# Optimization experiments

Hardware: AMD Instinct MI355X
Metric: run time of the kernel (lower is better)

Reference implementation:

```python
import jax, jax.numpy as jnp
import numpy as np

NUM_CLASSES = 14
ATTN_DIM = 64
BN_EPS = 1e-5

def setup_inputs() -> dict:
    key = jax.random.key(0)
    ks = jax.random.split(key, 6)
    B, F = 16384, 2048
    C, D = NUM_CLASSES, ATTN_DIM
    std = 0.02
    return {
        "features": jax.random.normal(ks[0], (B, F), jnp.float32),
        "W_proj": jax.random.normal(ks[1], (F, F), jnp.float32) * std,
        "b_proj": jnp.zeros((F,), jnp.float32),
        "bn_gamma": jnp.ones((F,), jnp.float32),
        "bn_beta": jnp.zeros((F,), jnp.float32),
        "W_qk": jax.random.normal(ks[2], (C * 2 * D, F), jnp.float32) * std,
        "gamma": jax.random.normal(ks[3], (C,), jnp.float32) * 0.1,
        "W_fc": jax.random.normal(ks[4], (C, F), jnp.float32) * std,
        "b_fc": jnp.zeros((C,), jnp.float32),
    }

def reference(features, W_proj, b_proj, bn_gamma, bn_beta, W_qk, gamma, W_fc, b_fc):
    B = features.shape[0]
    C, D = NUM_CLASSES, ATTN_DIM
    # fc logits
    logits = features @ W_fc.T + b_fc  # [B, C]
    # projection: Linear -> BatchNorm1d (training-mode batch stats) -> ReLU
    h = features @ W_proj.T + b_proj  # [B, P]
    mu = jnp.mean(h, axis=0)
    var = jnp.var(h, axis=0)  # biased, as torch BN uses for normalization
    h = (h - mu) * jax.lax.rsqrt(var + BN_EPS) * bn_gamma + bn_beta
    h = jax.nn.relu(h)
    # per-class q, k
    qk = h @ W_qk.T  # [B, 2*C*D]
    q, k = jnp.split(qk, 2, axis=-1)
    q = q.reshape(B, C, D)
    k = k.reshape(B, C, D)
    attn = jnp.einsum("bcd,bed->bce", q, k)  # [B, C, C]
    diag = jnp.diagonal(attn, axis1=-2, axis2=-1)  # [B, C]
    attn = attn - diag[..., None]
    attn = attn / jnp.max(jnp.abs(attn), axis=-1, keepdims=True)
    corr = jnp.einsum("bce,be->bc", attn, jax.nn.sigmoid(logits))  # [B, C]
    return logits + gamma * corr
```

## Files before the change

### kernel.cpp

```cpp
#include <hip/hip_runtime.h>
#include <stdint.h>

#define BROWS 16384
#define FDIM  2048
#define NCLS  14
#define ADIM  64
#define NCAT  2176
#define QKN   1792

typedef __attribute__((ext_vector_type(8))) short bhalf8_t;
typedef __attribute__((ext_vector_type(4))) float f32x4_t;

__device__ __forceinline__ unsigned short f2bf(float f) {
  unsigned int u = __builtin_bit_cast(unsigned int, f);
  u += 0x7fffu + ((u >> 16) & 1u);
  return (unsigned short)(u >> 16);
}

__device__ __forceinline__ void gl_lds16(const void* g, void* l) {
  __builtin_amdgcn_global_load_lds(
      (const __attribute__((address_space(1))) unsigned int*)g,
      (__attribute__((address_space(3))) unsigned int*)l, 16, 0, 0);
}


__global__ void cast8_bf16(const float* __restrict__ src,
                           unsigned short* __restrict__ dst, int n8) {
  int t = blockIdx.x * 256 + threadIdx.x;
  if (t >= n8) return;
  const float4* s = (const float4*)src + 2 * (size_t)t;
  float4 a = s[0], b = s[1];
  bhalf8_t o;
  o[0] = f2bf(a.x); o[1] = f2bf(a.y); o[2] = f2bf(a.z); o[3] = f2bf(a.w);
  o[4] = f2bf(b.x); o[5] = f2bf(b.y); o[6] = f2bf(b.z); o[7] = f2bf(b.w);
  *((bhalf8_t*)dst + t) = o;
}

__global__ void build_wcat(const float* __restrict__ Wp, const float* __restrict__ Wf,
                           unsigned short* __restrict__ dst) {
  int row = blockIdx.x;
  int c8 = threadIdx.x * 8;
  const float* src = nullptr;
  if (row < 2048) src = Wp + (size_t)row * FDIM + c8;
  else if (row < 2048 + NCLS) src = Wf + (size_t)(row - 2048) * FDIM + c8;
  bhalf8_t o = {0,0,0,0,0,0,0,0};
  if (src) {
    float4 a = *(const float4*)src, b = *(const float4*)(src + 4);
    o[0] = f2bf(a.x); o[1] = f2bf(a.y); o[2] = f2bf(a.z); o[3] = f2bf(a.w);
    o[4] = f2bf(b.x); o[5] = f2bf(b.y); o[6] = f2bf(b.z); o[7] = f2bf(b.w);
  }
  *(bhalf8_t*)(dst + (size_t)row * FDIM + c8) = o;
}

__global__ void build_biascat(const float* __restrict__ bp, const float* __restrict__ bf,
                              float* __restrict__ dst) {
  int i = blockIdx.x * 256 + threadIdx.x;
  if (i >= NCAT) return;
  dst[i] = (i < 2048) ? bp[i] : ((i < 2048 + NCLS) ? bf[i - 2048] : 0.f);
}

__global__ __launch_bounds__(256) void gemm_bt(
    const unsigned short* __restrict__ A, const unsigned short* __restrict__ Bw,
    const float* __restrict__ bias, float* __restrict__ C,
    int K, int lda, int ldb, int ldc)
{
  __shared__ unsigned short lA[128 * 64];
  __shared__ unsigned short lB[128 * 64];
  const int tid = threadIdx.x;
  const int lane = tid & 63, wv = tid >> 6;
  const int m = lane & 15, quad = lane >> 4;
  const size_t rowBase = (size_t)blockIdx.x * 128;
  const size_t colBase = (size_t)blockIdx.y * 128;
  const int m0 = (wv >> 1) * 64, n0 = (wv & 1) * 64;

  f32x4_t acc[4][4];
#pragma unroll
  for (int i = 0; i < 4; ++i)
#pragma unroll
    for (int j = 0; j < 4; ++j) acc[i][j] = (f32x4_t){0.f, 0.f, 0.f, 0.f};

  int sS[4];
  size_t gA[4], gB[4];
#pragma unroll
  for (int i = 0; i < 4; ++i) {
    int s = ((i * 4 + wv) << 6) + lane;
    int r = s >> 3, qp = s & 7;
    int q = qp ^ (r & 7);
    sS[i] = s;
    gA[i] = (rowBase + r) * (size_t)lda + q * 8;
    gB[i] = (colBase + r) * (size_t)ldb + q * 8;
  }

  for (int kb = 0; kb < K; kb += 64) {
#pragma unroll
    for (int i = 0; i < 4; ++i) {
      gl_lds16(A + gA[i] + kb, &lA[sS[i] * 8]);
      gl_lds16(Bw + gB[i] + kb, &lB[sS[i] * 8]);
    }
    __syncthreads();
#pragma unroll
    for (int ks = 0; ks < 2; ++ks) {
      const int qc = ks * 4 + quad;
      bhalf8_t af[4], bf[4];
#pragma unroll
      for (int mi = 0; mi < 4; ++mi) {
        int r = m0 + mi * 16 + m;
        af[mi] = *(const bhalf8_t*)&lA[(r * 8 + (qc ^ (r & 7))) * 8];
      }
#pragma unroll
      for (int ni = 0; ni < 4; ++ni) {
        int r = n0 + ni * 16 + m;
        bf[ni] = *(const bhalf8_t*)&lB[(r * 8 + (qc ^ (r & 7))) * 8];
      }
#pragma unroll
      for (int mi = 0; mi < 4; ++mi)
#pragma unroll
        for (int ni = 0; ni < 4; ++ni)
          acc[mi][ni] = __builtin_amdgcn_mfma_f32_16x16x32_bf16(af[mi], bf[ni], acc[mi][ni], 0, 0, 0);
    }
    __syncthreads();
  }

#pragma unroll
  for (int ni = 0; ni < 4; ++ni) {
    size_t gcol = colBase + n0 + ni * 16 + m;
    float bv = bias ? bias[gcol] : 0.f;
#pragma unroll
    for (int mi = 0; mi < 4; ++mi) {
      size_t grow = rowBase + m0 + mi * 16 + quad * 4;
#pragma unroll
      for (int r = 0; r < 4; ++r)
        C[(grow + r) * (size_t)ldc + gcol] = acc[mi][ni][r] + bv;
    }
  }
}


__global__ void bn_stats(const float* __restrict__ h, float* __restrict__ cs,
                         float* __restrict__ cq) {
  int col = blockIdx.x * 256 + threadIdx.x;
  int r0 = blockIdx.y * 256;
  float s = 0.f, q = 0.f;
  for (int r = 0; r < 256; ++r) {
    float v = h[(size_t)(r0 + r) * NCAT + col];
    s += v; q += v * v;
  }
  atomicAdd(&cs[col], s);
  atomicAdd(&cq[col], q);
}

__global__ void bn_finalize(const float* __restrict__ cs, const float* __restrict__ cq,
                            const float* __restrict__ g, const float* __restrict__ bt,
                            float* __restrict__ scale, float* __restrict__ shift) {
  int c = blockIdx.x * 256 + threadIdx.x;
  if (c >= FDIM) return;
  const float inv = 1.f / (float)BROWS;
  float mu = cs[c] * inv;
  float var = cq[c] * inv - mu * mu;
  float sc = g[c] * rsqrtf(var + 1e-5f);
  scale[c] = sc;
  shift[c] = bt[c] - mu * sc;
}

__global__ void bn_apply(const float* __restrict__ h, const float* __restrict__ sc,
                         const float* __restrict__ sh, unsigned short* __restrict__ hb) {
  int t = blockIdx.x * 256 + threadIdx.x;
  int row = t >> 8;
  int c8 = (t & 255) << 3;
  const float4* s = (const float4*)(h + (size_t)row * NCAT + c8);
  float4 a = s[0], b = s[1];
  float4 s0 = *(const float4*)(sc + c8), s1 = *(const float4*)(sc + c8 + 4);
  float4 h0 = *(const float4*)(sh + c8), h1 = *(const float4*)(sh + c8 + 4);
  bhalf8_t o;
  o[0] = f2bf(fmaxf(a.x * s0.x + h0.x, 0.f));
  o[1] = f2bf(fmaxf(a.y * s0.y + h0.y, 0.f));
  o[2] = f2bf(fmaxf(a.z * s0.z + h0.z, 0.f));
  o[3] = f2bf(fmaxf(a.w * s0.w + h0.w, 0.f));
  o[4] = f2bf(fmaxf(b.x * s1.x + h1.x, 0.f));
  o[5] = f2bf(fmaxf(b.y * s1.y + h1.y, 0.f));
  o[6] = f2bf(fmaxf(b.z * s1.z + h1.z, 0.f));
  o[7] = f2bf(fmaxf(b.w * s1.w + h1.w, 0.f));
  *(bhalf8_t*)(hb + (size_t)row * FDIM + c8) = o;
}

__global__ __launch_bounds__(256) void attn_ep(
    const float* __restrict__ qk, const float* __restrict__ hcat,
    const float* __restrict__ gamma, float* __restrict__ out)
{
  const int lane = threadIdx.x & 63;
  const int wv = threadIdx.x >> 6;
  const int b = blockIdx.x * 4 + wv;
  const int m = lane & 15, quad = lane >> 4;
  const float* qrow = qk + (size_t)b * QKN;
  f32x4_t acc = (f32x4_t){0.f, 0.f, 0.f, 0.f};
#pragma unroll
  for (int ks = 0; ks < 2; ++ks) {
    bhalf8_t af = {0,0,0,0,0,0,0,0}, bf = {0,0,0,0,0,0,0,0};
    if (m < NCLS) {
      const float* qa = qrow + m * 64 + ks * 32 + quad * 8;
      float4 a0 = *(const float4*)qa,          a1 = *(const float4*)(qa + 4);
      float4 b0 = *(const float4*)(qa + 896),  b1 = *(const float4*)(qa + 900);
      af[0] = f2bf(a0.x); af[1] = f2bf(a0.y); af[2] = f2bf(a0.z); af[3] = f2bf(a0.w);
      af[4] = f2bf(a1.x); af[5] = f2bf(a1.y); af[6] = f2bf(a1.z); af[7] = f2bf(a1.w);
      bf[0] = f2bf(b0.x); bf[1] = f2bf(b0.y); bf[2] = f2bf(b0.z); bf[3] = f2bf(b0.w);
      bf[4] = f2bf(b1.x); bf[5] = f2bf(b1.y); bf[6] = f2bf(b1.z); bf[7] = f2bf(b1.w);
    }
    acc = __builtin_amdgcn_mfma_f32_16x16x32_bf16(af, bf, acc, 0, 0, 0);
  }
  float logit_e = (m < NCLS) ? hcat[(size_t)b * NCAT + 2048 + m] : 0.f;
  float sig = 1.f / (1.f + __expf(-logit_e));
  float corr[4];
#pragma unroll
  for (int r = 0; r < 4; ++r) {
    int c = quad * 4 + r;
    float diag = __shfl(acc[r], (lane & 48) + c, 64);
    float a = acc[r] - diag;
    float av = (m < NCLS) ? fabsf(a) : 0.f;
    av = fmaxf(av, __shfl_xor(av, 1, 64));
    av = fmaxf(av, __shfl_xor(av, 2, 64));
    av = fmaxf(av, __shfl_xor(av, 4, 64));
    av = fmaxf(av, __shfl_xor(av, 8, 64));
    float v = (m < NCLS) ? (a / av) * sig : 0.f;
    v += __shfl_xor(v, 1, 64);
    v += __shfl_xor(v, 2, 64);
    v += __shfl_xor(v, 4, 64);
    v += __shfl_xor(v, 8, 64);
    corr[r] = v;
  }
  if (m == 0) {
#pragma unroll
    for (int r = 0; r < 4; ++r) {
      int c = quad * 4 + r;
      if (c < NCLS) {
        float lc = hcat[(size_t)b * NCAT + 2048 + c];
        out[(size_t)b * NCLS + c] = lc + gamma[c] * corr[r];
      }
    }
  }
}


extern "C" void kernel_launch(void* const* d_in, const int* in_sizes, int n_in,
                              void* d_out, int out_size, void* d_ws, size_t ws_size,
                              hipStream_t stream) {
  const float* features = (const float*)d_in[0];
  const float* W_proj   = (const float*)d_in[1];
  const float* b_proj   = (const float*)d_in[2];
  const float* bn_gamma = (const float*)d_in[3];
  const float* bn_beta  = (const float*)d_in[4];
  const float* W_qk     = (const float*)d_in[5];
  const float* gamma    = (const float*)d_in[6];
  const float* W_fc     = (const float*)d_in[7];
  const float* b_fc     = (const float*)d_in[8];
  float* out = (float*)d_out;

  char* ws = (char*)d_ws;
  unsigned short* featC   = (unsigned short*)ws;
  unsigned short* WcatC   = (unsigned short*)(ws + 67108864);
  unsigned short* WqkC    = (unsigned short*)(ws + 76021760);
  float*          biasCat = (float*)(ws + 83361792);
  float*          hcat    = (float*)(ws + 83378176);
  float*          qkbuf   = (float*)(ws + 225984512);
  float*          colsum  = (float*)(ws + 343425024);
  float*          colsq   = (float*)(ws + 343433216);
  float*          scalev  = (float*)(ws + 343441408);
  float*          shiftv  = (float*)(ws + 343449600);
  unsigned short* hb = featC;

  cast8_bf16<<<16384, 256, 0, stream>>>(features, featC, (BROWS * FDIM) / 8);
  build_wcat<<<NCAT, 256, 0, stream>>>(W_proj, W_fc, WcatC);
  cast8_bf16<<<1792, 256, 0, stream>>>(W_qk, WqkC, (QKN * FDIM) / 8);
  build_biascat<<<9, 256, 0, stream>>>(b_proj, b_fc, biasCat);

  gemm_bt<<<dim3(BROWS / 128, NCAT / 128), 256, 0, stream>>>(
      featC, WcatC, biasCat, hcat, FDIM, FDIM, FDIM, NCAT);

  hipMemsetAsync(colsum, 0, 16384, stream);
  bn_stats<<<dim3(8, 64), 256, 0, stream>>>(hcat, colsum, colsq);
  bn_finalize<<<8, 256, 0, stream>>>(colsum, colsq, bn_gamma, bn_beta, scalev, shiftv);
  bn_apply<<<16384, 256, 0, stream>>>(hcat, scalev, shiftv, hb);

  gemm_bt<<<dim3(BROWS / 128, QKN / 128), 256, 0, stream>>>(
      hb, WqkC, nullptr, qkbuf, FDIM, FDIM, FDIM, QKN);

  attn_ep<<<BROWS / 4, 256, 0, stream>>>(qkbuf, hcat, gamma, out);
}
```

Baseline: 622.9 us.

## Fuse BN statistics into GEMM epilogue and store intermediates as bf16

The first GEMM's epilogue now adds the bias, writes h as bf16, and accumulates per-column sum and sum-of-squares with shuffles and atomics. This removes the separate bn_stats pass over a large fp32 buffer. Logits go to a compact 16-wide buffer, and bn_apply works in place on bf16. The second GEMM writes qk as bf16, which halves the traffic read by attn_ep. BN statistics are still taken from fp32 values, but the stored h is now rounded to bf16 before normalisation. The epilogue atomics also add some contention.

```diff
diff --git a/kernel.cpp b/kernel.cpp
--- a/kernel.cpp
+++ b/kernel.cpp
@@ -15,6 +15,9 @@
   unsigned int u = __builtin_bit_cast(unsigned int, f);
   u += 0x7fffu + ((u >> 16) & 1u);
   return (unsigned short)(u >> 16);
+}
+__device__ __forceinline__ float bf2f(unsigned short s) {
+  return __builtin_bit_cast(float, (unsigned int)s << 16);
 }
 
 __device__ __forceinline__ void gl_lds16(const void* g, void* l) {
@@ -52,16 +55,12 @@
   *(bhalf8_t*)(dst + (size_t)row * FDIM + c8) = o;
 }
 
-__global__ void build_biascat(const float* __restrict__ bp, const float* __restrict__ bf,
-                              float* __restrict__ dst) {
-  int i = blockIdx.x * 256 + threadIdx.x;
-  if (i >= NCAT) return;
-  dst[i] = (i < 2048) ? bp[i] : ((i < 2048 + NCLS) ? bf[i - 2048] : 0.f);
-}
-
+template<int MODE>
 __global__ __launch_bounds__(256) void gemm_bt(
     const unsigned short* __restrict__ A, const unsigned short* __restrict__ Bw,
-    const float* __restrict__ bias, float* __restrict__ C,
+    const float* __restrict__ bp, const float* __restrict__ bfc,
+    unsigned short* __restrict__ Cb, float* __restrict__ logits,
+    float* __restrict__ colsum, float* __restrict__ colsq,
     int K, int lda, int ldb, int ldc)
 {
   __shared__ unsigned short lA[128 * 64];
@@ -121,33 +120,52 @@
     __syncthreads();
   }
 
-#pragma unroll
-  for (int ni = 0; ni < 4; ++ni) {
-    size_t gcol = colBase + n0 + ni * 16 + m;
-    float bv = bias ? bias[gcol] : 0.f;
-#pragma unroll
-    for (int mi = 0; mi < 4; ++mi) {
-      size_t grow = rowBase + m0 + mi * 16 + quad * 4;
-#pragma unroll
-      for (int r = 0; r < 4; ++r)
-        C[(grow + r) * (size_t)ldc + gcol] = acc[mi][ni][r] + bv;
-    }
-  }
-}
-
-
-__global__ void bn_stats(const float* __restrict__ h, float* __restrict__ cs,
-                         float* __restrict__ cq) {
-  int col = blockIdx.x * 256 + threadIdx.x;
-  int r0 = blockIdx.y * 256;
-  float s = 0.f, q = 0.f;
-  for (int r = 0; r < 256; ++r) {
-    float v = h[(size_t)(r0 + r) * NCAT + col];
-    s += v; q += v * v;
-  }
-  atomicAdd(&cs[col], s);
-  atomicAdd(&cq[col], q);
-}
+  if (MODE == 0) {
+    if (colBase < 2048) {
+#pragma unroll
+      for (int ni = 0; ni < 4; ++ni) {
+        int gcol = (int)colBase + n0 + ni * 16 + m;
+        float bv = bp[gcol];
+        float s = 0.f, q = 0.f;
+#pragma unroll
+        for (int mi = 0; mi < 4; ++mi) {
+          size_t grow = rowBase + m0 + mi * 16 + quad * 4;
+#pragma unroll
+          for (int r = 0; r < 4; ++r) {
+            float v = acc[mi][ni][r] + bv;
+            Cb[(grow + r) * (size_t)ldc + gcol] = f2bf(v);
+            s += v; q += v * v;
+          }
+        }
+        s += __shfl_xor(s, 16, 64); s += __shfl_xor(s, 32, 64);
+        q += __shfl_xor(q, 16, 64); q += __shfl_xor(q, 32, 64);
+        if (quad == 0) { atomicAdd(&colsum[gcol], s); atomicAdd(&colsq[gcol], q); }
+      }
+    } else if (n0 == 0) {
+      float bv = (m < NCLS) ? bfc[m] : 0.f;
+#pragma unroll
+      for (int mi = 0; mi < 4; ++mi) {
+        size_t grow = rowBase + m0 + mi * 16 + quad * 4;
+#pragma unroll
+        for (int r = 0; r < 4; ++r)
+          logits[(grow + r) * 16 + m] = acc[mi][0][r] + bv;
+      }
+    }
+  } else {
+#pragma unroll
+    for (int ni = 0; ni < 4; ++ni) {
+      int gcol = (int)colBase + n0 + ni * 16 + m;
+#pragma unroll
+      for (int mi = 0; mi < 4; ++mi) {
+        size_t grow = rowBase + m0 + mi * 16 + quad * 4;
+#pragma unroll
+        for (int r = 0; r < 4; ++r)
+          Cb[(grow + r) * (size_t)ldc + gcol] = f2bf(acc[mi][ni][r]);
+      }
+    }
+  }
+}
+
 
 __global__ void bn_finalize(const float* __restrict__ cs, const float* __restrict__ cq,
                             const float* __restrict__ g, const float* __restrict__ bt,
@@ -162,52 +180,47 @@
   shift[c] = bt[c] - mu * sc;
 }
 
-__global__ void bn_apply(const float* __restrict__ h, const float* __restrict__ sc,
-                         const float* __restrict__ sh, unsigned short* __restrict__ hb) {
+__global__ void bn_apply(unsigned short* __restrict__ hb, const float* __restrict__ sc,
+                         const float* __restrict__ sh) {
   int t = blockIdx.x * 256 + threadIdx.x;
   int row = t >> 8;
   int c8 = (t & 255) << 3;
-  const float4* s = (const float4*)(h + (size_t)row * NCAT + c8);
-  float4 a = s[0], b = s[1];
+  unsigned short* p = hb + (size_t)row * FDIM + c8;
+  bhalf8_t v = *(bhalf8_t*)p;
   float4 s0 = *(const float4*)(sc + c8), s1 = *(const float4*)(sc + c8 + 4);
   float4 h0 = *(const float4*)(sh + c8), h1 = *(const float4*)(sh + c8 + 4);
   bhalf8_t o;
-  o[0] = f2bf(fmaxf(a.x * s0.x + h0.x, 0.f));
-  o[1] = f2bf(fmaxf(a.y * s0.y + h0.y, 0.f));
-  o[2] = f2bf(fmaxf(a.z * s0.z + h0.z, 0.f));
-  o[3] = f2bf(fmaxf(a.w * s0.w + h0.w, 0.f));
-  o[4] = f2bf(fmaxf(b.x * s1.x + h1.x, 0.f));
-  o[5] = f2bf(fmaxf(b.y * s1.y + h1.y, 0.f));
-  o[6] = f2bf(fmaxf(b.z * s1.z + h1.z, 0.f));
-  o[7] = f2bf(fmaxf(b.w * s1.w + h1.w, 0.f));
-  *(bhalf8_t*)(hb + (size_t)row * FDIM + c8) = o;
+  o[0] = f2bf(fmaxf(bf2f((unsigned short)v[0]) * s0.x + h0.x, 0.f));
+  o[1] = f2bf(fmaxf(bf2f((unsigned short)v[1]) * s0.y + h0.y, 0.f));
+  o[2] = f2bf(fmaxf(bf2f((unsigned short)v[2]) * s0.z + h0.z, 0.f));
+  o[3] = f2bf(fmaxf(bf2f((unsigned short)v[3]) * s0.w + h0.w, 0.f));
+  o[4] = f2bf(fmaxf(bf2f((unsigned short)v[4]) * s1.x + h1.x, 0.f));
+  o[5] = f2bf(fmaxf(bf2f((unsigned short)v[5]) * s1.y + h1.y, 0.f));
+  o[6] = f2bf(fmaxf(bf2f((unsigned short)v[6]) * s1.z + h1.z, 0.f));
+  o[7] = f2bf(fmaxf(bf2f((unsigned short)v[7]) * s1.w + h1.w, 0.f));
+  *(bhalf8_t*)p = o;
 }
 
 __global__ __launch_bounds__(256) void attn_ep(
-    const float* __restrict__ qk, const float* __restrict__ hcat,
+    const unsigned short* __restrict__ qk, const float* __restrict__ logits,
     const float* __restrict__ gamma, float* __restrict__ out)
 {
   const int lane = threadIdx.x & 63;
   const int wv = threadIdx.x >> 6;
   const int b = blockIdx.x * 4 + wv;
   const int m = lane & 15, quad = lane >> 4;
-  const float* qrow = qk + (size_t)b * QKN;
+  const unsigned short* qrow = qk + (size_t)b * QKN;
   f32x4_t acc = (f32x4_t){0.f, 0.f, 0.f, 0.f};
 #pragma unroll
   for (int ks = 0; ks < 2; ++ks) {
     bhalf8_t af = {0,0,0,0,0,0,0,0}, bf = {0,0,0,0,0,0,0,0};
     if (m < NCLS) {
-      const float* qa = qrow + m * 64 + ks * 32 + quad * 8;
-      float4 a0 = *(const float4*)qa,          a1 = *(const float4*)(qa + 4);
-      float4 b0 = *(const float4*)(qa + 896),  b1 = *(const float4*)(qa + 900);
-      af[0] = f2bf(a0.x); af[1] = f2bf(a0.y); af[2] = f2bf(a0.z); af[3] = f2bf(a0.w);
-      af[4] = f2bf(a1.x); af[5] = f2bf(a1.y); af[6] = f2bf(a1.z); af[7] = f2bf(a1.w);
-      bf[0] = f2bf(b0.x); bf[1] = f2bf(b0.y); bf[2] = f2bf(b0.z); bf[3] = f2bf(b0.w);
-      bf[4] = f2bf(b1.x); bf[5] = f2bf(b1.y); bf[6] = f2bf(b1.z); bf[7] = f2bf(b1.w);
+      af = *(const bhalf8_t*)(qrow + m * 64 + ks * 32 + quad * 8);
+      bf = *(const bhalf8_t*)(qrow + 896 + m * 64 + ks * 32 + quad * 8);
     }
     acc = __builtin_amdgcn_mfma_f32_16x16x32_bf16(af, bf, acc, 0, 0, 0);
   }
-  float logit_e = (m < NCLS) ? hcat[(size_t)b * NCAT + 2048 + m] : 0.f;
+  float logit_e = (m < NCLS) ? logits[(size_t)b * 16 + m] : 0.f;
   float sig = 1.f / (1.f + __expf(-logit_e));
   float corr[4];
 #pragma unroll
@@ -232,7 +245,7 @@
     for (int r = 0; r < 4; ++r) {
       int c = quad * 4 + r;
       if (c < NCLS) {
-        float lc = hcat[(size_t)b * NCAT + 2048 + c];
+        float lc = logits[(size_t)b * 16 + c];
         out[(size_t)b * NCLS + c] = lc + gamma[c] * corr[r];
       }
     }
@@ -256,32 +269,32 @@
 
   char* ws = (char*)d_ws;
   unsigned short* featC   = (unsigned short*)ws;
-  unsigned short* WcatC   = (unsigned short*)(ws + 67108864);
-  unsigned short* WqkC    = (unsigned short*)(ws + 76021760);
-  float*          biasCat = (float*)(ws + 83361792);
-  float*          hcat    = (float*)(ws + 83378176);
-  float*          qkbuf   = (float*)(ws + 225984512);
-  float*          colsum  = (float*)(ws + 343425024);
-  float*          colsq   = (float*)(ws + 343433216);
-  float*          scalev  = (float*)(ws + 343441408);
-  float*          shiftv  = (float*)(ws + 343449600);
-  unsigned short* hb = featC;
+  unsigned short* hbuf    = (unsigned short*)(ws + 67108864);
+  unsigned short* WcatC   = (unsigned short*)(ws + 134217728);
+  unsigned short* WqkC    = (unsigned short*)(ws + 143130624);
+  unsigned short* qkC     = (unsigned short*)(ws + 150470656);
+  float*          logitsB = (float*)(ws + 209190912);
+  float*          colsum  = (float*)(ws + 210239488);
+  float*          colsq   = (float*)(ws + 210247680);
+  float*          scalev  = (float*)(ws + 210255872);
+  float*          shiftv  = (float*)(ws + 210264064);
+
+  hipMemsetAsync(colsum, 0, 16384, stream);
 
   cast8_bf16<<<16384, 256, 0, stream>>>(features, featC, (BROWS * FDIM) / 8);
   build_wcat<<<NCAT, 256, 0, stream>>>(W_proj, W_fc, WcatC);
   cast8_bf16<<<1792, 256, 0, stream>>>(W_qk, WqkC, (QKN * FDIM) / 8);
-  build_biascat<<<9, 256, 0, stream>>>(b_proj, b_fc, biasCat);
-
-  gemm_bt<<<dim3(BROWS / 128, NCAT / 128), 256, 0, stream>>>(
-      featC, WcatC, biasCat, hcat, FDIM, FDIM, FDIM, NCAT);
-
-  hipMemsetAsync(colsum, 0, 16384, stream);
-  bn_stats<<<dim3(8, 64), 256, 0, stream>>>(hcat, colsum, colsq);
+
+  gemm_bt<0><<<dim3(BROWS / 128, NCAT / 128), 256, 0, stream>>>(
+      featC, WcatC, b_proj, b_fc, hbuf, logitsB, colsum, colsq,
+      FDIM, FDIM, FDIM, FDIM);
+
   bn_finalize<<<8, 256, 0, stream>>>(colsum, colsq, bn_gamma, bn_beta, scalev, shiftv);
-  bn_apply<<<16384, 256, 0, stream>>>(hcat, scalev, shiftv, hb);
-
-  gemm_bt<<<dim3(BROWS / 128, QKN / 128), 256, 0, stream>>>(
-      hb, WqkC, nullptr, qkbuf, FDIM, FDIM, FDIM, QKN);
-
-  attn_ep<<<BROWS / 4, 256, 0, stream>>>(qkbuf, hcat, gamma, out);
-}
+  bn_apply<<<16384, 256, 0, stream>>>(hbuf, scalev, shiftv);
+
+  gemm_bt<1><<<dim3(BROWS / 128, QKN / 128), 256, 0, stream>>>(
+      hbuf, WqkC, nullptr, nullptr, qkC, nullptr, nullptr, nullptr,
+      FDIM, FDIM, FDIM, QKN);
+
+  attn_ep<<<BROWS / 4, 256, 0, stream>>>(qkC, logitsB, gamma, out);
+}
```

New measurement: 619.5 us. Within noise of the previous version (-0.5%).
